# Kernel tuning notes

Hardware: AMD Instinct MI355X
Metric: run time of the kernel (lower is better)

The kernel has to match this reference:

```python
import jax, jax.numpy as jnp
import numpy as np
import math

D_MODEL = 512
N_HEADS = 2
B, S = 2, 1024
THRESHOLD = 0.5  # kwargs default 'sparsity_threshold'


def setup_inputs() -> dict:
    key = jax.random.key(0)
    ks = jax.random.split(key, 10)
    D, H = D_MODEL, D_MODEL // 4
    std = 0.02
    return {
        "x": jax.random.normal(ks[0], (B, S, D), jnp.float32),
        "Wq": jax.random.normal(ks[1], (D, D), jnp.float32) * std,
        "Wk": jax.random.normal(ks[2], (D, D), jnp.float32) * std,
        "Wv": jax.random.normal(ks[3], (D, D), jnp.float32) * std,
        "Wo": jax.random.normal(ks[4], (D, D), jnp.float32) * std,
        "bo": jnp.zeros((D,), jnp.float32),
        "W1": jax.random.normal(ks[5], (D, H), jnp.float32) * std,
        "b1": jnp.zeros((H,), jnp.float32),
        "W2": jax.random.normal(ks[6], (H, 1), jnp.float32) * std,
        "b2": jnp.zeros((1,), jnp.float32),
    }


def reference(x, Wq, Wk, Wv, Wo, bo, W1, b1, W2, b2):
    Bsz, Seq, D = x.shape
    Hn = N_HEADS
    dh = D // Hn

    def split_heads(t):
        return t.reshape(Bsz, Seq, Hn, dh).transpose(0, 2, 1, 3)  # [B,H,S,dh]

    q = split_heads(x @ Wq)
    k = split_heads(x @ Wk)
    v = split_heads(x @ Wv)

    scores = jnp.einsum("bhid,bhjd->bhij", q, k) / math.sqrt(dh)  # [B,H,S,S]

    # head-mean features for the pairwise sparsity predictor (n_heads==2 => 2*dh == D)
    q_mean = q.mean(axis=1)  # [B,S,dh]
    k_mean = k.mean(axis=1)  # [B,S,dh]
    # Linear1 of cat([q_mean_i, k_mean_j]) splits into two halves of W1
    a = q_mean @ W1[:dh]   # [B,S,Dh4]
    c = k_mean @ W1[dh:]   # [B,S,Dh4]
    hidden = jax.nn.relu(a[:, :, None, :] + c[:, None, :, :] + b1)  # [B,S,S,Dh4]
    connection_probs = jax.nn.sigmoid(jnp.squeeze(hidden @ W2, -1) + b2[0])  # [B,S,S]

    mask = connection_probs > THRESHOLD  # [B,S,S]
    scores = jnp.where(mask[:, None, :, :], scores, jnp.float32(-1e9))
    attn = jax.nn.softmax(scores, axis=-1)  # dropout inactive in eval

    out = jnp.einsum("bhij,bhjd->bhid", attn, v)  # [B,H,S,dh]
    out = out.transpose(0, 2, 1, 3).reshape(Bsz, Seq, D)
    out = out @ Wo + bo
    return out
```

## Files before the change

### kernel.cpp

```cpp
#include <hip/hip_runtime.h>


typedef unsigned short u16t;
typedef __bf16 bf16x8 __attribute__((ext_vector_type(8)));
typedef float f32x4 __attribute__((ext_vector_type(4)));

#define B_SZ 2
#define S_SZ 1024
#define D_SZ 512
#define DH 256
#define HH 128

static __device__ __forceinline__ u16t f2b(float f) {
    unsigned int u = __builtin_bit_cast(unsigned int, f);
    u += 0x7FFFu + ((u >> 16) & 1u);
    return (u16t)(u >> 16);
}

static __device__ __forceinline__ f32x4 mfma16(bf16x8 a, bf16x8 b, f32x4 c) {
    return __builtin_amdgcn_mfma_f32_16x16x32_bf16(a, b, c, 0, 0, 0);
}

static __device__ __forceinline__ void gload16(const void* g, void* l) {
    __builtin_amdgcn_global_load_lds(
        (const __attribute__((address_space(1))) void*)g,
        (__attribute__((address_space(3))) void*)l, 16, 0, 0);
}

__global__ __launch_bounds__(256) void k_prep(
    const float* __restrict__ x,
    const float* __restrict__ Wq, const float* __restrict__ Wk,
    const float* __restrict__ Wv, const float* __restrict__ Wo,
    const float* __restrict__ W1,
    u16t* __restrict__ xb, u16t* __restrict__ WT, float* __restrict__ Beff)
{
    __shared__ float smf[1088];
    int bidx = blockIdx.x;
    int t = threadIdx.x;
    if (bidx < 1024) {
        int idx = (bidx * 256 + t) * 4;
        float4 v = *(const float4*)(x + idx);
        u16t* o = xb + idx;
        o[0] = f2b(v.x); o[1] = f2b(v.y); o[2] = f2b(v.z); o[3] = f2b(v.w);
    } else if (bidx < 2048) {
        int t2 = bidx - 1024;
        int z = t2 >> 8, rem = t2 & 255;
        int n0 = (rem & 15) * 32, k0 = (rem >> 4) * 32;
        const float* W = z == 0 ? Wq : z == 1 ? Wk : z == 2 ? Wv : Wo;
        u16t* WTz = WT + (size_t)z * D_SZ * D_SZ;
        float (*tile)[33] = (float(*)[33])smf;
        int r = t >> 3, c4 = (t & 7) * 4;
        float4 v = *(const float4*)(W + (size_t)(k0 + r) * D_SZ + n0 + c4);
        tile[r][c4] = v.x; tile[r][c4 + 1] = v.y; tile[r][c4 + 2] = v.z; tile[r][c4 + 3] = v.w;
        __syncthreads();
        u16t o[4];
        o[0] = f2b(tile[c4][r]); o[1] = f2b(tile[c4 + 1][r]);
        o[2] = f2b(tile[c4 + 2][r]); o[3] = f2b(tile[c4 + 3][r]);
        *(ushort4*)(WTz + (size_t)(n0 + r) * D_SZ + k0 + c4) = *(ushort4*)o;
    } else {
        int k = bidx - 2048;
        float* wm0 = smf;
        float* wm1 = smf + 256;
        const float* wrq = Wq + (size_t)k * D_SZ;
        const float* wrk = Wk + (size_t)k * D_SZ;
        wm0[t & 255] = 0.5f * (wrq[t & 255] + wrq[(t & 255) + DH]);
        wm1[t & 255] = 0.5f * (wrk[t & 255] + wrk[(t & 255) + DH]);
        __syncthreads();
        int half = t >> 7, hcol = t & 127;
        const float* wm = half ? wm1 : wm0;
        const float* W1h = W1 + (half ? (size_t)DH * HH : 0);
        float s = 0.f;
        for (int d = 0; d < 256; ++d) s += wm[d] * W1h[(size_t)d * HH + hcol];
        Beff[(size_t)k * 256 + half * 128 + hcol] = s;
    }
}

template<int MF, int NF>
static __device__ __forceinline__ void gemm_db(
    const u16t* __restrict__ A, int lda, const u16t* __restrict__ B, int ldb,
    int K, int tid, u16t* Als, u16t* Bls, f32x4 acc[MF][NF])
{
    const int w = tid >> 6, lane = tid & 63;
    const int lr = lane & 15, kg = lane >> 4;
    const int srow = lane >> 3, scol = (lane & 7) * 8;
    const int ABUF = MF * 4096;
    const int BBUF = NF * 1024;
    auto stage = [&](int bb, int k0) {
#pragma unroll
        for (int q = 0; q < MF * 2; ++q) {
            int ci = w * (MF * 2) + q;
            gload16(A + (size_t)(ci * 8 + srow) * lda + k0 + scol,
                    Als + bb * ABUF + ci * 512);
        }
#pragma unroll
        for (int q = 0; q < NF / 2; ++q) {
            int cj = w * (NF / 2) + q;
            gload16(B + (size_t)(cj * 8 + srow) * ldb + k0 + scol,
                    Bls + bb * BBUF + cj * 512);
        }
    };
    stage(0, 0);
    __syncthreads();
    const int nt = K / 64;
    for (int t = 0; t < nt; ++t) {
        int cur = t & 1;
        if (t + 1 < nt) stage(cur ^ 1, (t + 1) * 64);
        const u16t* Ab = Als + cur * ABUF;
        const u16t* Bb = Bls + cur * BBUF;
#pragma unroll
        for (int kk = 0; kk < 2; ++kk) {
            bf16x8 af[MF], bfr[NF];
#pragma unroll
            for (int fi = 0; fi < MF; ++fi)
                af[fi] = *(const bf16x8*)(&Ab[(w * (MF * 16) + fi * 16 + lr) * 64 + kk * 32 + kg * 8]);
#pragma unroll
            for (int fj = 0; fj < NF; ++fj)
                bfr[fj] = *(const bf16x8*)(&Bb[(fj * 16 + lr) * 64 + kk * 32 + kg * 8]);
#pragma unroll
            for (int fi = 0; fi < MF; ++fi)
#pragma unroll
                for (int fj = 0; fj < NF; ++fj)
                    acc[fi][fj] = mfma16(af[fi], bfr[fj], acc[fi][fj]);
        }
        __syncthreads();
    }
}


__global__ __launch_bounds__(256) void k_qkvac(
    const u16t* __restrict__ xb, const u16t* __restrict__ WT,
    const float* __restrict__ x, const float* __restrict__ Beff,
    const float* __restrict__ b1,
    u16t* __restrict__ qb, u16t* __restrict__ kb, u16t* __restrict__ vT,
    float* __restrict__ a, float* __restrict__ cc)
{
    __shared__ __align__(16) char sm[49152];
    int bid = blockIdx.x;
    int t = threadIdx.x;
    if (bid < 384) {
        u16t* Als = (u16t*)sm;
        u16t* Bls = (u16t*)(sm + 32768);
        int z = bid / 128, rem = bid & 127;
        int m0 = (rem >> 3) * 128, n0 = (rem & 7) * 64;
        const u16t* A = xb + (size_t)m0 * D_SZ;
        const u16t* Bt = WT + (size_t)z * D_SZ * D_SZ + (size_t)n0 * D_SZ;
        f32x4 acc[2][4] = {};
        gemm_db<2, 4>(A, D_SZ, Bt, D_SZ, D_SZ, t, Als, Bls, acc);
        int w = t >> 6, lane = t & 63, lr = lane & 15, kg = lane >> 4;
        if (z < 2) {
            u16t (*vls)[68] = (u16t(*)[68])sm;
            float scale = z == 0 ? 0.0625f : 1.0f;
#pragma unroll
            for (int fi = 0; fi < 2; ++fi)
#pragma unroll
                for (int fj = 0; fj < 4; ++fj)
#pragma unroll
                    for (int rr = 0; rr < 4; ++rr)
                        vls[w * 32 + fi * 16 + kg * 4 + rr][fj * 16 + lr]
                            = f2b(acc[fi][fj][rr] * scale);
            __syncthreads();
            u16t* dst = z == 0 ? qb : kb;
            int c8 = (t & 7) * 8, r0 = t >> 3;
#pragma unroll
            for (int p = 0; p < 4; ++p) {
                int r = r0 + p * 32;
                *(uint4*)(dst + (size_t)(m0 + r) * D_SZ + n0 + c8) = *(const uint4*)(&vls[r][c8]);
            }
        } else {
            u16t (*vls)[136] = (u16t(*)[136])sm;
#pragma unroll
            for (int fi = 0; fi < 2; ++fi)
#pragma unroll
                for (int fj = 0; fj < 4; ++fj)
#pragma unroll
                    for (int rr = 0; rr < 4; ++rr)
                        vls[fj * 16 + lr][w * 32 + fi * 16 + kg * 4 + rr] = f2b(acc[fi][fj][rr]);
            __syncthreads();
            int b = m0 >> 10, s0 = m0 & 1023;
            int cr = t >> 2, seg = t & 3;
            const u16t* srcp = &vls[cr][seg * 32];
            u16t* dstp = vT + (((size_t)(b * D_SZ + n0 + cr)) << 10) + s0 + seg * 32;
#pragma unroll
            for (int qq = 0; qq < 4; ++qq)
                *(uint4*)(dstp + qq * 8) = *(const uint4*)(srcp + qq * 8);
        }
    } else {
        float (*xs)[68] = (float(*)[68])sm;
        float (*bsT)[68] = (float(*)[68])(sm + 17408);
        int t2 = bid - 384;
        int r0 = (t2 & 31) * 64, n0 = (t2 >> 5) * 32;
        int ti = t >> 4, tj = t & 15;
        float acc[4][2] = {};
        for (int k0 = 0; k0 < 512; k0 += 64) {
            if (k0) __syncthreads();
#pragma unroll
            for (int p = 0; p < 4; ++p) {
                int idx = t + p * 256;
                int r = idx >> 4, c4 = (idx & 15) * 4;
                *(float4*)&xs[r][c4] = *(const float4*)(x + (size_t)(r0 + r) * D_SZ + k0 + c4);
            }
#pragma unroll
            for (int p = 0; p < 2; ++p) {
                int idx = t + p * 256;
                int k = idx >> 3, n4 = (idx & 7) * 4;
                float4 v = *(const float4*)(Beff + (size_t)(k0 + k) * 256 + n0 + n4);
                bsT[n4][k] = v.x; bsT[n4 + 1][k] = v.y; bsT[n4 + 2][k] = v.z; bsT[n4 + 3][k] = v.w;
            }
            __syncthreads();
#pragma unroll
            for (int kk = 0; kk < 16; ++kk) {
                float4 xv[4], bv[2];
#pragma unroll
                for (int ri = 0; ri < 4; ++ri) xv[ri] = *(const float4*)&xs[ti + 16 * ri][kk * 4];
#pragma unroll
                for (int rj = 0; rj < 2; ++rj) bv[rj] = *(const float4*)&bsT[tj + 16 * rj][kk * 4];
#pragma unroll
                for (int ri = 0; ri < 4; ++ri)
#pragma unroll
                    for (int rj = 0; rj < 2; ++rj)
                        acc[ri][rj] += xv[ri].x * bv[rj].x + xv[ri].y * bv[rj].y
                                     + xv[ri].z * bv[rj].z + xv[ri].w * bv[rj].w;
            }
        }
        bool isA = n0 < 128;
#pragma unroll
        for (int rj = 0; rj < 2; ++rj) {
            int col = n0 + tj + 16 * rj;
            float badd = isA ? b1[col] : 0.f;
#pragma unroll
            for (int ri = 0; ri < 4; ++ri) {
                int row = r0 + ti + 16 * ri;
                if (isA) a[(size_t)row * HH + col] = acc[ri][rj] + badd;
                else     cc[(size_t)row * HH + (col - 128)] = acc[ri][rj];
            }
        }
    }
}

__global__ __launch_bounds__(256) void k_scores(
    const u16t* __restrict__ qb, const u16t* __restrict__ kb,
    const float* __restrict__ a, const float* __restrict__ c,
    const float* __restrict__ W2, const float* __restrict__ b2,
    u16t* __restrict__ P, float* __restrict__ lpart)
{
    __shared__ __align__(16) char sm[55296];
    float (*at)[132] = (float(*)[132])sm;
    float (*ct)[132] = (float(*)[132])(sm + 33792);
    unsigned char (*msk)[64] = (unsigned char(*)[64])(sm + 50688);
    float* w2s = (float*)(sm + 54784);
    int b = blockIdx.z, mt = blockIdx.y, jb = blockIdx.x;
    int m0 = mt * 64, j0 = jb * 64;
    int t = threadIdx.x;
    if (t < 128) w2s[t] = W2[t];
#pragma unroll
    for (int p = 0; p < 8; ++p) {
        int idx = t + p * 256;
        int r = idx >> 5, c4 = (idx & 31) * 4;
        *(float4*)&at[r][c4] = *(const float4*)(a + ((size_t)(b * S_SZ + m0 + r)) * HH + c4);
    }
    float fb2 = b2[0];
    int ti = t >> 4, tj = t & 15;
#pragma unroll
    for (int jh = 0; jh < 2; ++jh) {
        __syncthreads();
#pragma unroll
        for (int p = 0; p < 4; ++p) {
            int idx = t + p * 256;
            int r = idx >> 5, c4 = (idx & 31) * 4;
            *(float4*)&ct[r][c4] =
                *(const float4*)(c + ((size_t)(b * S_SZ + j0 + jh * 32 + r)) * HH + c4);
        }
        __syncthreads();
        float accm[4][2];
#pragma unroll
        for (int ri = 0; ri < 4; ++ri)
#pragma unroll
            for (int rj = 0; rj < 2; ++rj) accm[ri][rj] = fb2;
#pragma unroll 2
        for (int h4 = 0; h4 < 32; ++h4) {
            float4 wv = ((const float4*)w2s)[h4];
            float4 av[4], cv[2];
#pragma unroll
            for (int ri = 0; ri < 4; ++ri) av[ri] = *(const float4*)&at[ti + 16 * ri][h4 * 4];
#pragma unroll
            for (int rj = 0; rj < 2; ++rj) cv[rj] = *(const float4*)&ct[tj + 16 * rj][h4 * 4];
#pragma unroll
            for (int ri = 0; ri < 4; ++ri)
#pragma unroll
                for (int rj = 0; rj < 2; ++rj) {
                    accm[ri][rj] += fmaxf(av[ri].x + cv[rj].x, 0.f) * wv.x;
                    accm[ri][rj] += fmaxf(av[ri].y + cv[rj].y, 0.f) * wv.y;
                    accm[ri][rj] += fmaxf(av[ri].z + cv[rj].z, 0.f) * wv.z;
                    accm[ri][rj] += fmaxf(av[ri].w + cv[rj].w, 0.f) * wv.w;
                }
        }
#pragma unroll
        for (int ri = 0; ri < 4; ++ri)
#pragma unroll
            for (int rj = 0; rj < 2; ++rj)
                msk[ti + 16 * ri][jh * 32 + tj + 16 * rj] = accm[ri][rj] > 0.f ? 1 : 0;
    }
    __syncthreads();
    u16t* Als = (u16t*)sm;
    u16t* Bls = (u16t*)(sm + 16384);
    const u16t* A = qb + (size_t)(b * S_SZ + m0) * D_SZ;
    const u16t* B = kb + (size_t)(b * S_SZ + j0) * D_SZ;
    const int w = t >> 6, lane = t & 63, lr = lane & 15, kg = lane >> 4;
    const int srow = lane >> 3, scol = (lane & 7) * 8;
    auto stage = [&](int bb, int k0) {
#pragma unroll
        for (int q = 0; q < 2; ++q) {
            int ci = w * 2 + q;
            gload16(A + (size_t)(ci * 8 + srow) * D_SZ + k0 + scol, Als + bb * 4096 + ci * 512);
            gload16(B + (size_t)(ci * 8 + srow) * D_SZ + k0 + scol, Bls + bb * 4096 + ci * 512);
        }
    };
    f32x4 acc0[4] = {}, acc1[4] = {};
    stage(0, 0);
    __syncthreads();
#pragma unroll
    for (int t8 = 0; t8 < 8; ++t8) {
        int cur = t8 & 1;
        if (t8 < 7) stage(cur ^ 1, (t8 + 1) * 64);
        const u16t* Ab = Als + cur * 4096;
        const u16t* Bb = Bls + cur * 4096;
#pragma unroll
        for (int kk = 0; kk < 2; ++kk) {
            bf16x8 af = *(const bf16x8*)(&Ab[(w * 16 + lr) * 64 + kk * 32 + kg * 8]);
            bf16x8 bfr[4];
#pragma unroll
            for (int fj = 0; fj < 4; ++fj)
                bfr[fj] = *(const bf16x8*)(&Bb[(fj * 16 + lr) * 64 + kk * 32 + kg * 8]);
            if (t8 < 4) {
#pragma unroll
                for (int fj = 0; fj < 4; ++fj) acc0[fj] = mfma16(af, bfr[fj], acc0[fj]);
            } else {
#pragma unroll
                for (int fj = 0; fj < 4; ++fj) acc1[fj] = mfma16(af, bfr[fj], acc1[fj]);
            }
        }
        __syncthreads();
    }
    u16t (*vls)[68] = (u16t(*)[68])sm;
#pragma unroll
    for (int h = 0; h < 2; ++h) {
#pragma unroll
        for (int rr = 0; rr < 4; ++rr) {
            int il = w * 16 + kg * 4 + rr;
            float rs = 0.f;
#pragma unroll
            for (int fj = 0; fj < 4; ++fj) {
                int jl = fj * 16 + lr;
                float s = h ? acc1[fj][rr] : acc0[fj][rr];
                float e = msk[il][jl] ? __expf(s) : 0.f;
                if (h) acc1[fj][rr] = e; else acc0[fj][rr] = e;
                rs += e;
            }
            rs += __shfl_xor(rs, 1); rs += __shfl_xor(rs, 2);
            rs += __shfl_xor(rs, 4); rs += __shfl_xor(rs, 8);
            if (lr == 0)
                lpart[((size_t)(jb * 4 + b * 2 + h) << 10) + m0 + il] = rs;
        }
#pragma unroll
        for (int fj = 0; fj < 4; ++fj)
#pragma unroll
            for (int rr = 0; rr < 4; ++rr)
                vls[w * 16 + kg * 4 + rr][fj * 16 + lr]
                    = f2b(h ? acc1[fj][rr] : acc0[fj][rr]);
        __syncthreads();
        int r = t >> 2, c16 = (t & 3) * 16;
        u16t* dstp = P + ((size_t)(b * 2 + h) << 20) + ((size_t)(m0 + r) << 10) + j0 + c16;
        *(uint4*)dstp = *(const uint4*)(&vls[r][c16]);
        *(uint4*)(dstp + 8) = *(const uint4*)(&vls[r][c16 + 8]);
        __syncthreads();
    }
}

__global__ __launch_bounds__(256) void k_pv(
    const u16t* __restrict__ P, const u16t* __restrict__ vT,
    const float* __restrict__ lpart, u16t* __restrict__ ao)
{
    __shared__ __align__(16) u16t sm[12288];
    __shared__ float invl[64];
    u16t* Als = sm;
    u16t* Bls = sm + 8192;
    int bh = blockIdx.z, b = bh >> 1, h = bh & 1;
    int m0 = blockIdx.y * 64, n0 = blockIdx.x * 32;
    int t = threadIdx.x;
    if (t < 64) {
        float l = 0.f;
        for (int jb = 0; jb < 16; ++jb)
            l += lpart[((size_t)(jb * 4 + bh) << 10) + m0 + t];
        invl[t] = l > 0.f ? 1.0f / l : 0.f;
    }
    const u16t* A = P + ((size_t)bh << 20) + (size_t)m0 * S_SZ;
    const u16t* Bt = vT + ((size_t)(b * D_SZ + h * DH + n0)) * S_SZ;
    f32x4 acc[1][2] = {};
    gemm_db<1, 2>(A, S_SZ, Bt, S_SZ, S_SZ, t, Als, Bls, acc);
    int w = t >> 6, lane = t & 63, lr = lane & 15, kg = lane >> 4;
    u16t (*ols)[40] = (u16t(*)[40])sm;
#pragma unroll
    for (int fj = 0; fj < 2; ++fj)
#pragma unroll
        for (int rr = 0; rr < 4; ++rr) {
            int rl = w * 16 + kg * 4 + rr;
            ols[rl][fj * 16 + lr] = f2b(acc[0][fj][rr] * invl[rl]);
        }
    __syncthreads();
    int r = t >> 2, c8 = (t & 3) * 8;
    *(uint4*)(ao + ((size_t)(b * S_SZ + m0 + r)) * D_SZ + h * DH + n0 + c8)
        = *(const uint4*)(&ols[r][c8]);
}

__global__ __launch_bounds__(256) void k_out(
    const u16t* __restrict__ ao, const u16t* __restrict__ WoT,
    const float* __restrict__ bo, float* __restrict__ out)
{
    __shared__ __align__(16) u16t sm[12288];
    u16t* Als = sm;
    u16t* Bls = sm + 8192;
    int m0 = blockIdx.y * 64, n0 = blockIdx.x * 32;
    const u16t* A = ao + (size_t)m0 * D_SZ;
    const u16t* Bt = WoT + (size_t)n0 * D_SZ;
    f32x4 acc[1][2] = {};
    gemm_db<1, 2>(A, D_SZ, Bt, D_SZ, D_SZ, threadIdx.x, Als, Bls, acc);
    int w = threadIdx.x >> 6, lane = threadIdx.x & 63, lr = lane & 15, kg = lane >> 4;
    float (*ols)[36] = (float(*)[36])sm;
#pragma unroll
    for (int fj = 0; fj < 2; ++fj)
#pragma unroll
        for (int rr = 0; rr < 4; ++rr) {
            int rl = w * 16 + kg * 4 + rr;
            ols[rl][fj * 16 + lr] = acc[0][fj][rr] + bo[n0 + fj * 16 + lr];
        }
    __syncthreads();
    int r0 = threadIdx.x >> 3, c4 = (threadIdx.x & 7) * 4;
#pragma unroll
    for (int p = 0; p < 2; ++p) {
        int r = r0 + p * 32;
        *(float4*)(out + (size_t)(m0 + r) * D_SZ + n0 + c4) = *(const float4*)(&ols[r][c4]);
    }
}

extern "C" void kernel_launch(void* const* d_in, const int* in_sizes, int n_in,
                              void* d_out, int out_size, void* d_ws, size_t ws_size,
                              hipStream_t stream)
{
    const float* x  = (const float*)d_in[0];
    const float* Wq = (const float*)d_in[1];
    const float* Wk = (const float*)d_in[2];
    const float* Wv = (const float*)d_in[3];
    const float* Wo = (const float*)d_in[4];
    const float* bo = (const float*)d_in[5];
    const float* W1 = (const float*)d_in[6];
    const float* b1 = (const float*)d_in[7];
    const float* W2 = (const float*)d_in[8];
    const float* b2 = (const float*)d_in[9];
    float* out = (float*)d_out;

    char* ws = (char*)d_ws;
    size_t off = 0;
    auto carve = [&](size_t bytes) { void* p = ws + off; off += (bytes + 255) & ~(size_t)255; return p; };
    u16t* xb   = (u16t*)carve((size_t)2048 * 512 * 2);
    u16t* WT   = (u16t*)carve((size_t)4 * 512 * 512 * 2);
    u16t* qb   = (u16t*)carve((size_t)2048 * 512 * 2);
    u16t* kb   = (u16t*)carve((size_t)2048 * 512 * 2);
    u16t* vT   = (u16t*)carve((size_t)2 * 512 * 1024 * 2);
    float* Beff = (float*)carve((size_t)512 * 256 * 4);
    float* a   = (float*)carve((size_t)2048 * 128 * 4);
    float* c   = (float*)carve((size_t)2048 * 128 * 4);
    u16t* P    = (u16t*)carve((size_t)4 * 1024 * 1024 * 2);
    float* lpart = (float*)carve((size_t)16 * 4 * 1024 * 4);
    u16t* ao   = (u16t*)carve((size_t)2048 * 512 * 2);
    (void)ws_size;

    k_prep<<<dim3(2560), dim3(256), 0, stream>>>(x, Wq, Wk, Wv, Wo, W1, xb, WT, Beff);
    k_qkvac<<<dim3(640), dim3(256), 0, stream>>>(xb, WT, x, Beff, b1, qb, kb, vT, a, c);
    k_scores<<<dim3(16, 16, 2), dim3(256), 0, stream>>>(qb, kb, a, c, W2, b2, P, lpart);
    k_pv<<<dim3(8, 16, 4), dim3(256), 0, stream>>>(P, vT, lpart, ao);
    k_out<<<dim3(16, 32), dim3(256), 0, stream>>>(ao, WT + (size_t)3 * 512 * 512, bo, out);
}
```

Measured before the change: 103.2 us.

## Shrink QKV GEMM tiles and restructure mask predictor to cut LDS footprint

The QKV projection tiles are halved from 128x64 to 64x64, doubling the block count from 384 to 768. This shrinks shared memory from 48KB to 32KB, so more blocks run per CU and the grid better fills the GPU. In k_scores, the pairwise-MLP mask computation now streams the hidden dimension in chunks of 32 for both a and c, and each thread handles a 4x4 register tile instead of two 4x2 passes. This cuts LDS from about 54KB to 36KB and reuses each loaded value across more outputs. The trade-offs are more syncthreads, more global reloads of a, and more accumulator registers per thread.

```diff
diff --git a/kernel.cpp b/kernel.cpp
--- a/kernel.cpp
+++ b/kernel.cpp
@@ -134,60 +134,55 @@
     u16t* __restrict__ qb, u16t* __restrict__ kb, u16t* __restrict__ vT,
     float* __restrict__ a, float* __restrict__ cc)
 {
-    __shared__ __align__(16) char sm[49152];
+    __shared__ __align__(16) char sm[32768];
     int bid = blockIdx.x;
     int t = threadIdx.x;
-    if (bid < 384) {
+    if (bid < 768) {
         u16t* Als = (u16t*)sm;
-        u16t* Bls = (u16t*)(sm + 32768);
-        int z = bid / 128, rem = bid & 127;
-        int m0 = (rem >> 3) * 128, n0 = (rem & 7) * 64;
+        u16t* Bls = (u16t*)(sm + 16384);
+        int z = bid >> 8, rem = bid & 255;
+        int m0 = (rem >> 3) * 64, n0 = (rem & 7) * 64;
         const u16t* A = xb + (size_t)m0 * D_SZ;
         const u16t* Bt = WT + (size_t)z * D_SZ * D_SZ + (size_t)n0 * D_SZ;
-        f32x4 acc[2][4] = {};
-        gemm_db<2, 4>(A, D_SZ, Bt, D_SZ, D_SZ, t, Als, Bls, acc);
+        f32x4 acc[1][4] = {};
+        gemm_db<1, 4>(A, D_SZ, Bt, D_SZ, D_SZ, t, Als, Bls, acc);
         int w = t >> 6, lane = t & 63, lr = lane & 15, kg = lane >> 4;
         if (z < 2) {
             u16t (*vls)[68] = (u16t(*)[68])sm;
             float scale = z == 0 ? 0.0625f : 1.0f;
 #pragma unroll
-            for (int fi = 0; fi < 2; ++fi)
-#pragma unroll
-                for (int fj = 0; fj < 4; ++fj)
-#pragma unroll
-                    for (int rr = 0; rr < 4; ++rr)
-                        vls[w * 32 + fi * 16 + kg * 4 + rr][fj * 16 + lr]
-                            = f2b(acc[fi][fj][rr] * scale);
+            for (int fj = 0; fj < 4; ++fj)
+#pragma unroll
+                for (int rr = 0; rr < 4; ++rr)
+                    vls[w * 16 + kg * 4 + rr][fj * 16 + lr]
+                        = f2b(acc[0][fj][rr] * scale);
             __syncthreads();
             u16t* dst = z == 0 ? qb : kb;
             int c8 = (t & 7) * 8, r0 = t >> 3;
 #pragma unroll
-            for (int p = 0; p < 4; ++p) {
+            for (int p = 0; p < 2; ++p) {
                 int r = r0 + p * 32;
                 *(uint4*)(dst + (size_t)(m0 + r) * D_SZ + n0 + c8) = *(const uint4*)(&vls[r][c8]);
             }
         } else {
-            u16t (*vls)[136] = (u16t(*)[136])sm;
-#pragma unroll
-            for (int fi = 0; fi < 2; ++fi)
-#pragma unroll
-                for (int fj = 0; fj < 4; ++fj)
-#pragma unroll
-                    for (int rr = 0; rr < 4; ++rr)
-                        vls[fj * 16 + lr][w * 32 + fi * 16 + kg * 4 + rr] = f2b(acc[fi][fj][rr]);
+            u16t (*vls)[72] = (u16t(*)[72])sm;
+#pragma unroll
+            for (int fj = 0; fj < 4; ++fj)
+#pragma unroll
+                for (int rr = 0; rr < 4; ++rr)
+                    vls[fj * 16 + lr][w * 16 + kg * 4 + rr] = f2b(acc[0][fj][rr]);
             __syncthreads();
             int b = m0 >> 10, s0 = m0 & 1023;
             int cr = t >> 2, seg = t & 3;
-            const u16t* srcp = &vls[cr][seg * 32];
-            u16t* dstp = vT + (((size_t)(b * D_SZ + n0 + cr)) << 10) + s0 + seg * 32;
-#pragma unroll
-            for (int qq = 0; qq < 4; ++qq)
-                *(uint4*)(dstp + qq * 8) = *(const uint4*)(srcp + qq * 8);
+            const u16t* srcp = &vls[cr][seg * 16];
+            u16t* dstp = vT + (((size_t)(b * D_SZ + n0 + cr)) << 10) + s0 + seg * 16;
+            *(uint4*)dstp = *(const uint4*)srcp;
+            *(uint4*)(dstp + 8) = *(const uint4*)(srcp + 8);
         }
     } else {
         float (*xs)[68] = (float(*)[68])sm;
         float (*bsT)[68] = (float(*)[68])(sm + 17408);
-        int t2 = bid - 384;
+        int t2 = bid - 768;
         int r0 = (t2 & 31) * 64, n0 = (t2 >> 5) * 32;
         int ti = t >> 4, tj = t & 15;
         float acc[4][2] = {};
@@ -243,63 +238,56 @@
     const float* __restrict__ W2, const float* __restrict__ b2,
     u16t* __restrict__ P, float* __restrict__ lpart)
 {
-    __shared__ __align__(16) char sm[55296];
-    float (*at)[132] = (float(*)[132])sm;
-    float (*ct)[132] = (float(*)[132])(sm + 33792);
-    unsigned char (*msk)[64] = (unsigned char(*)[64])(sm + 50688);
-    float* w2s = (float*)(sm + 54784);
+    __shared__ __align__(16) char sm[36864];
+    float (*at)[36] = (float(*)[36])sm;
+    float (*ct)[36] = (float(*)[36])(sm + 9216);
+    float* w2s = (float*)(sm + 18432);
+    unsigned char (*msk)[64] = (unsigned char(*)[64])(sm + 32768);
     int b = blockIdx.z, mt = blockIdx.y, jb = blockIdx.x;
     int m0 = mt * 64, j0 = jb * 64;
     int t = threadIdx.x;
     if (t < 128) w2s[t] = W2[t];
-#pragma unroll
-    for (int p = 0; p < 8; ++p) {
-        int idx = t + p * 256;
-        int r = idx >> 5, c4 = (idx & 31) * 4;
-        *(float4*)&at[r][c4] = *(const float4*)(a + ((size_t)(b * S_SZ + m0 + r)) * HH + c4);
-    }
     float fb2 = b2[0];
     int ti = t >> 4, tj = t & 15;
-#pragma unroll
-    for (int jh = 0; jh < 2; ++jh) {
-        __syncthreads();
-#pragma unroll
-        for (int p = 0; p < 4; ++p) {
-            int idx = t + p * 256;
-            int r = idx >> 5, c4 = (idx & 31) * 4;
-            *(float4*)&ct[r][c4] =
-                *(const float4*)(c + ((size_t)(b * S_SZ + j0 + jh * 32 + r)) * HH + c4);
-        }
-        __syncthreads();
-        float accm[4][2];
-#pragma unroll
-        for (int ri = 0; ri < 4; ++ri)
-#pragma unroll
-            for (int rj = 0; rj < 2; ++rj) accm[ri][rj] = fb2;
-#pragma unroll 2
-        for (int h4 = 0; h4 < 32; ++h4) {
-            float4 wv = ((const float4*)w2s)[h4];
-            float4 av[4], cv[2];
+    float accm[4][4];
+#pragma unroll
+    for (int ri = 0; ri < 4; ++ri)
+#pragma unroll
+        for (int rj = 0; rj < 4; ++rj) accm[ri][rj] = fb2;
+    int sr = t >> 2, sc = (t & 3) * 8;
+    for (int hc = 0; hc < 4; ++hc) {
+        __syncthreads();
+        const float* ap = a + (size_t)(b * S_SZ + m0 + sr) * HH + hc * 32 + sc;
+        const float* cp = c + (size_t)(b * S_SZ + j0 + sr) * HH + hc * 32 + sc;
+        *(float4*)&at[sr][sc]     = *(const float4*)ap;
+        *(float4*)&at[sr][sc + 4] = *(const float4*)(ap + 4);
+        *(float4*)&ct[sr][sc]     = *(const float4*)cp;
+        *(float4*)&ct[sr][sc + 4] = *(const float4*)(cp + 4);
+        __syncthreads();
+#pragma unroll
+        for (int h4 = 0; h4 < 8; ++h4) {
+            float4 wv = *(const float4*)&w2s[hc * 32 + h4 * 4];
+            float4 av[4], cv[4];
 #pragma unroll
             for (int ri = 0; ri < 4; ++ri) av[ri] = *(const float4*)&at[ti + 16 * ri][h4 * 4];
 #pragma unroll
-            for (int rj = 0; rj < 2; ++rj) cv[rj] = *(const float4*)&ct[tj + 16 * rj][h4 * 4];
+            for (int rj = 0; rj < 4; ++rj) cv[rj] = *(const float4*)&ct[tj + 16 * rj][h4 * 4];
 #pragma unroll
             for (int ri = 0; ri < 4; ++ri)
 #pragma unroll
-                for (int rj = 0; rj < 2; ++rj) {
+                for (int rj = 0; rj < 4; ++rj) {
                     accm[ri][rj] += fmaxf(av[ri].x + cv[rj].x, 0.f) * wv.x;
                     accm[ri][rj] += fmaxf(av[ri].y + cv[rj].y, 0.f) * wv.y;
                     accm[ri][rj] += fmaxf(av[ri].z + cv[rj].z, 0.f) * wv.z;
                     accm[ri][rj] += fmaxf(av[ri].w + cv[rj].w, 0.f) * wv.w;
                 }
         }
-#pragma unroll
-        for (int ri = 0; ri < 4; ++ri)
-#pragma unroll
-            for (int rj = 0; rj < 2; ++rj)
-                msk[ti + 16 * ri][jh * 32 + tj + 16 * rj] = accm[ri][rj] > 0.f ? 1 : 0;
-    }
+    }
+#pragma unroll
+    for (int ri = 0; ri < 4; ++ri)
+#pragma unroll
+        for (int rj = 0; rj < 4; ++rj)
+            msk[ti + 16 * ri][tj + 16 * rj] = accm[ri][rj] > 0.f ? 1 : 0;
     __syncthreads();
     u16t* Als = (u16t*)sm;
     u16t* Bls = (u16t*)(sm + 16384);
@@ -475,7 +463,7 @@
     (void)ws_size;
 
     k_prep<<<dim3(2560), dim3(256), 0, stream>>>(x, Wq, Wk, Wv, Wo, W1, xb, WT, Beff);
-    k_qkvac<<<dim3(640), dim3(256), 0, stream>>>(xb, WT, x, Beff, b1, qb, kb, vT, a, c);
+    k_qkvac<<<dim3(1024), dim3(256), 0, stream>>>(xb, WT, x, Beff, b1, qb, kb, vT, a, c);
     k_scores<<<dim3(16, 16, 2), dim3(256), 0, stream>>>(qb, kb, a, c, W2, b2, P, lpart);
     k_pv<<<dim3(8, 16, 4), dim3(256), 0, stream>>>(P, vT, lpart, ao);
     k_out<<<dim3(16, 32), dim3(256), 0, stream>>>(ao, WT + (size_t)3 * 512 * 512, bo, out);
```

Result: slower. 111.5 us (+8.1%).
